# Kernel optimization log

Measured on AMD Instinct MI355X. Metric: run time of the kernel, lower is better.

Reference implementation:

```python
import jax, jax.numpy as jnp
import numpy as np
from jax import lax


def setup_inputs() -> dict:
    key = jax.random.key(0)
    ks = jax.random.split(key, 6)
    B = 32768
    P, C, F = 20, 10, 4 * 14 * 14
    x = jax.random.normal(ks[0], (B, 1, 28, 28), dtype=jnp.float32)
    conv_w = jax.random.normal(ks[1], (4, 1, 2, 2), dtype=jnp.float32) * 0.5
    conv_b = jax.random.normal(ks[2], (4,), dtype=jnp.float32) * 0.1
    prototypes = jax.random.normal(ks[3], (P, F), dtype=jnp.float32)
    cls_w = jax.random.normal(ks[4], (C, P), dtype=jnp.float32) * (1.0 / np.sqrt(P))
    cls_b = jax.random.normal(ks[5], (C,), dtype=jnp.float32) * 0.1
    return {"x": x, "conv_w": conv_w, "conv_b": conv_b,
            "prototypes": prototypes, "cls_w": cls_w, "cls_b": cls_b}


def reference(x, conv_w, conv_b, prototypes, cls_w, cls_b):
    # QuanvolutionFilter: Conv2d(1,4,k=2,s=2) -> [B,4,14,14] -> flatten [B,784]
    feats = lax.conv_general_dilated(
        x, conv_w, window_strides=(2, 2), padding="VALID",
        dimension_numbers=("NCHW", "OIHW", "NCHW"))
    feats = feats + conv_b[None, :, None, None]
    features = feats.reshape(x.shape[0], -1)  # [B, 784]

    # QuantumKernel: x.reshape(1,-1) collapses batch; only indices 0..3 are read.
    # RY(x_i) then RY(-y_i) per wire => |0000> amplitude = prod_i cos((x_i-y_i)/2).
    x4 = features.reshape(-1)[:4]                    # [4]
    p4 = prototypes[:, :4]                           # [P,4]
    k = jnp.abs(jnp.prod(jnp.cos((x4[None, :] - p4) * 0.5), axis=1))  # [P]

    logits = k[None, :] @ cls_w.T + cls_b            # [1, C]
    return jax.nn.log_softmax(logits, axis=-1)
```

## Files before the change

kernel.cpp:

```cpp
#include <hip/hip_runtime.h>
#include <math.h>


__global__ void HybridQuanvolution_kernel(const float* __restrict__ x,
                                          const float* __restrict__ conv_w,
                                          const float* __restrict__ conv_b,
                                          const float* __restrict__ prototypes,
                                          const float* __restrict__ cls_w,
                                          const float* __restrict__ cls_b,
                                          float* __restrict__ out) {
    __shared__ float k_sh[20];
    __shared__ float logits_sh[10];
    const int t = threadIdx.x;

    if (t < 20) {
        const float w00 = conv_w[0], w01 = conv_w[1];
        const float w10 = conv_w[2], w11 = conv_w[3];
        const float b0  = conv_b[0];
        float k = 1.0f;
        #pragma unroll
        for (int j = 0; j < 4; ++j) {
            const float x4 = x[2 * j] * w00 + x[2 * j + 1] * w01 +
                             x[28 + 2 * j] * w10 + x[28 + 2 * j + 1] * w11 + b0;
            const float d = (x4 - prototypes[t * 784 + j]) * 0.5f;
            k *= cosf(d);
        }
        k_sh[t] = fabsf(k);
    }
    __syncthreads();

    if (t < 10) {
        float acc = cls_b[t];
        #pragma unroll
        for (int p = 0; p < 20; ++p) acc += k_sh[p] * cls_w[t * 20 + p];
        logits_sh[t] = acc;
    }
    __syncthreads();

    if (t < 10) {
        float m = -INFINITY;
        #pragma unroll
        for (int c = 0; c < 10; ++c) m = fmaxf(m, logits_sh[c]);
        float s = 0.0f;
        #pragma unroll
        for (int c = 0; c < 10; ++c) s += expf(logits_sh[c] - m);
        out[t] = logits_sh[t] - m - logf(s);
    }
}

extern "C" void kernel_launch(void* const* d_in, const int* in_sizes, int n_in,
                              void* d_out, int out_size, void* d_ws, size_t ws_size,
                              hipStream_t stream) {
    const float* x          = (const float*)d_in[0];
    const float* conv_w     = (const float*)d_in[1];
    const float* conv_b     = (const float*)d_in[2];
    const float* prototypes = (const float*)d_in[3];
    const float* cls_w      = (const float*)d_in[4];
    const float* cls_b      = (const float*)d_in[5];
    float* out = (float*)d_out;

    HybridQuanvolution_kernel<<<1, 64, 0, stream>>>(x, conv_w, conv_b, prototypes,
                                                    cls_w, cls_b, out);
}
```

Measured before the change: 9.645 us.

## Replace shared memory and barriers with wave shuffles and hoisted vector loads

Moves all global loads (x patch, conv weights, prototype rows, classifier rows) to the top of the kernel as float4 loads so they are issued together and their latency overlaps. The shared-memory staging and two __syncthreads are replaced with wave-level __shfl broadcasts for the classifier dot product and the softmax reduction. This targets the serialized load latency and barrier overhead of a tiny single-block kernel that is dominated by launch and latency costs. It relies on the 64-thread block being exactly one wavefront and on the float4 alignment of the inputs.

```diff
diff --git a/kernel.cpp b/kernel.cpp
--- a/kernel.cpp
+++ b/kernel.cpp
@@ -2,50 +2,69 @@
 #include <math.h>
 
 
-__global__ void HybridQuanvolution_kernel(const float* __restrict__ x,
-                                          const float* __restrict__ conv_w,
-                                          const float* __restrict__ conv_b,
-                                          const float* __restrict__ prototypes,
-                                          const float* __restrict__ cls_w,
-                                          const float* __restrict__ cls_b,
-                                          float* __restrict__ out) {
-    __shared__ float k_sh[20];
-    __shared__ float logits_sh[10];
+__global__ void __launch_bounds__(64)
+HybridQuanvolution_kernel(const float* __restrict__ x,
+                          const float* __restrict__ conv_w,
+                          const float* __restrict__ conv_b,
+                          const float* __restrict__ prototypes,
+                          const float* __restrict__ cls_w,
+                          const float* __restrict__ cls_b,
+                          float* __restrict__ out) {
     const int t = threadIdx.x;
 
+    const float4 cwv = *reinterpret_cast<const float4*>(conv_w);
+    const float  b0  = conv_b[0];
+    const float4 xa = *reinterpret_cast<const float4*>(x);
+    const float4 xb = *reinterpret_cast<const float4*>(x + 4);
+    const float4 xc = *reinterpret_cast<const float4*>(x + 28);
+    const float4 xd = *reinterpret_cast<const float4*>(x + 32);
+
+    float4 pv = make_float4(0.f, 0.f, 0.f, 0.f);
+    if (t < 20)
+        pv = *reinterpret_cast<const float4*>(prototypes + t * 784);
+
+    float wv[20];
+    #pragma unroll
+    for (int i = 0; i < 20; ++i) wv[i] = 0.f;
+    float bv = 0.f;
+    if (t < 10) {
+        #pragma unroll
+        for (int i = 0; i < 5; ++i)
+            reinterpret_cast<float4*>(wv)[i] =
+                reinterpret_cast<const float4*>(cls_w + t * 20)[i];
+        bv = cls_b[t];
+    }
+
+    const float r0[8] = {xa.x, xa.y, xa.z, xa.w, xb.x, xb.y, xb.z, xb.w};
+    const float r1[8] = {xc.x, xc.y, xc.z, xc.w, xd.x, xd.y, xd.z, xd.w};
+    const float pj[4] = {pv.x, pv.y, pv.z, pv.w};
+    float k = 0.f;
     if (t < 20) {
-        const float w00 = conv_w[0], w01 = conv_w[1];
-        const float w10 = conv_w[2], w11 = conv_w[3];
-        const float b0  = conv_b[0];
-        float k = 1.0f;
+        float prod = 1.f;
         #pragma unroll
         for (int j = 0; j < 4; ++j) {
-            const float x4 = x[2 * j] * w00 + x[2 * j + 1] * w01 +
-                             x[28 + 2 * j] * w10 + x[28 + 2 * j + 1] * w11 + b0;
-            const float d = (x4 - prototypes[t * 784 + j]) * 0.5f;
-            k *= cosf(d);
+            const float x4 = r0[2 * j] * cwv.x + r0[2 * j + 1] * cwv.y +
+                             r1[2 * j] * cwv.z + r1[2 * j + 1] * cwv.w + b0;
+            prod *= cosf((x4 - pj[j]) * 0.5f);
         }
-        k_sh[t] = fabsf(k);
+        k = fabsf(prod);
     }
-    __syncthreads();
 
-    if (t < 10) {
-        float acc = cls_b[t];
-        #pragma unroll
-        for (int p = 0; p < 20; ++p) acc += k_sh[p] * cls_w[t * 20 + p];
-        logits_sh[t] = acc;
-    }
-    __syncthreads();
+    float acc = bv;
+    #pragma unroll
+    for (int p = 0; p < 20; ++p) acc += __shfl(k, p) * wv[p];
 
-    if (t < 10) {
-        float m = -INFINITY;
-        #pragma unroll
-        for (int c = 0; c < 10; ++c) m = fmaxf(m, logits_sh[c]);
-        float s = 0.0f;
-        #pragma unroll
-        for (int c = 0; c < 10; ++c) s += expf(logits_sh[c] - m);
-        out[t] = logits_sh[t] - m - logf(s);
-    }
+    float lg[10];
+    #pragma unroll
+    for (int c = 0; c < 10; ++c) lg[c] = __shfl(acc, c);
+    float m = -INFINITY;
+    #pragma unroll
+    for (int c = 0; c < 10; ++c) m = fmaxf(m, lg[c]);
+    float s = 0.f;
+    #pragma unroll
+    for (int c = 0; c < 10; ++c) s += expf(lg[c] - m);
+
+    if (t < 10) out[t] = acc - m - logf(s);
 }
 
 extern "C" void kernel_launch(void* const* d_in, const int* in_sizes, int n_in,
```

Result: slower. 10.44 us (+8.3%).
